# Optimization experiments

Hardware: AMD Instinct MI355X
Metric: run time of the kernel (lower is better)

The kernel has to match this reference:

```python
import jax, jax.numpy as jnp
import numpy as np

K = 20  # max_similar_relations


def setup_inputs() -> dict:
    key = jax.random.key(0)
    k1, k2 = jax.random.split(key)
    B, R, D = 256, 2048, 64
    x = jax.random.normal(k1, (B, R, D), dtype=jnp.float32)
    query_rels = jax.random.randint(k2, (B,), 0, R, dtype=jnp.int32)
    return {
        "x": x,
        "query_rels": query_rels,
        # raw params as in __init__: threshold_init=0.2 -> raw=0.2*2-1=-0.6; strength_init=0.05 -> raw=0.05*5-1=-0.75
        "threshold_raw": jnp.float32(-0.6),
        "strength_raw": jnp.float32(-0.75),
        "weight_scale": jnp.float32(1.0),
        "temperature": jnp.float32(1.0),
    }


def reference(x, query_rels, threshold_raw, strength_raw, weight_scale, temperature):
    B, R, D = x.shape
    bidx = jnp.arange(B)
    threshold = jax.nn.sigmoid(threshold_raw)
    strength = jax.nn.sigmoid(strength_raw) * 0.2
    temp = jnp.clip(temperature, 0.1, 10.0)

    # F.normalize(x, p=2, dim=2)
    norms = x / jnp.maximum(jnp.linalg.norm(x, axis=2, keepdims=True), 1e-12)

    q = norms[bidx, query_rels]                      # [B, D] normalized query reprs
    sims = jnp.einsum("bd,brd->br", q, norms)        # [B, R] cosine similarities
    sims = sims.at[bidx, query_rels].set(-1.0)       # exclude self
    sim_w = jax.nn.sigmoid((sims - threshold) * 10.0)

    topv, topi = jax.lax.top_k(sims, K)              # [B, K]
    valid = (topv > threshold) & (topi != query_rels[:, None])

    # softmax over valid top-k entries only (per batch row)
    logits = jnp.where(valid, topv / temp, -1e9)
    w = jax.nn.softmax(logits, axis=1)
    w = jnp.where(valid, w, 0.0)

    sw = jnp.take_along_axis(sim_w, topi, axis=1)    # smooth sigmoid weights of selected
    combined = w * sw
    adjusted = combined * (1.0 + weight_scale * topv)
    adjusted = adjusted / (jnp.sum(adjusted, axis=1, keepdims=True) + 1e-8)

    # gather top-k normalized reprs and weighted-sum them
    top_reprs = jnp.take_along_axis(norms, jnp.broadcast_to(topi[:, :, None], (B, K, D)), axis=1)
    weighted = jnp.einsum("bk,bkd->bd", adjusted, top_reprs)  # [B, D]

    q_orig = x[bidx, query_rels]                     # original (unnormalized) query repr
    has_valid = jnp.any(valid, axis=1, keepdims=True)
    mixed = (1.0 - strength) * q_orig + strength * weighted
    new_q = jnp.where(has_valid, mixed, q_orig)

    return x.at[bidx, query_rels].set(new_q)
```

## Files before the change

### kernel.cpp

```cpp
#include <hip/hip_runtime.h>
#include <math.h>

#define KTOP 20
#define R_MAX 2048
#define SPLIT 8

typedef float f4v __attribute__((ext_vector_type(4)));

__global__ __launch_bounds__(256, 6) void stream_sims(
    const float* __restrict__ x,
    const int* __restrict__ qrels,
    float* __restrict__ out,
    float* __restrict__ sims,
    float* __restrict__ dns,
    int R)
{
    __shared__ float s_q[64];
    const int blk = blockIdx.x;
    const int b = blk >> 3;
    const int s = blk & (SPLIT - 1);
    const int t = threadIdx.x;
    const int qr = qrels[b];
    const long xbase = (long)b * R * 64;

    if (t < 64) {
        float v = x[xbase + (long)qr * 64 + t];
        float ss = v * v;
#pragma unroll
        for (int m = 1; m < 64; m <<= 1) ss += __shfl_xor(ss, m, 64);
        s_q[t] = v / fmaxf(sqrtf(ss), 1e-12f);
    }
    __syncthreads();

    const int grp = t >> 4, l16 = t & 15;
    const float4 q4 = *(const float4*)(s_q + l16 * 4);
    const int rpb = R / SPLIT;
    const int row0 = s * rpb;
    const long sbase = (long)b * R;

    for (int r = row0 + grp; r < row0 + rpb; r += 32) {
        const int rA = r, rB = r + 16;
        const long baseA = xbase + (long)rA * 64 + l16 * 4;
        const long baseB = xbase + (long)rB * 64 + l16 * 4;
        const float4 vA = *(const float4*)(x + baseA);
        const float4 vB = *(const float4*)(x + baseB);
        __builtin_nontemporal_store(*(const f4v*)&vA, (f4v*)(out + baseA));
        __builtin_nontemporal_store(*(const f4v*)&vB, (f4v*)(out + baseB));

        float dotA = vA.x * q4.x + vA.y * q4.y + vA.z * q4.z + vA.w * q4.w;
        float ssA  = vA.x * vA.x + vA.y * vA.y + vA.z * vA.z + vA.w * vA.w;
        float dotB = vB.x * q4.x + vB.y * q4.y + vB.z * q4.z + vB.w * q4.w;
        float ssB  = vB.x * vB.x + vB.y * vB.y + vB.z * vB.z + vB.w * vB.w;
#pragma unroll
        for (int m = 1; m < 16; m <<= 1) {
            dotA += __shfl_xor(dotA, m, 64);
            ssA  += __shfl_xor(ssA,  m, 64);
            dotB += __shfl_xor(dotB, m, 64);
            ssB  += __shfl_xor(ssB,  m, 64);
        }
        if (l16 == 0) {
            float dnA = fmaxf(sqrtf(ssA), 1e-12f);
            float dnB = fmaxf(sqrtf(ssB), 1e-12f);
            sims[sbase + rA] = (rA == qr) ? -1.0f : dotA / dnA;
            sims[sbase + rB] = (rB == qr) ? -1.0f : dotB / dnB;
            dns[sbase + rA] = dnA;
            dns[sbase + rB] = dnB;
        }
    }
}

__global__ __launch_bounds__(256) void select_mix(
    const float* __restrict__ x,
    const int* __restrict__ qrels,
    const float* __restrict__ thr_raw,
    const float* __restrict__ str_raw,
    const float* __restrict__ wscale_p,
    const float* __restrict__ temp_p,
    const float* __restrict__ sims,
    const float* __restrict__ dns,
    float* __restrict__ out,
    int R)
{
    __shared__ float s_sims[R_MAX];
    __shared__ int   s_cand[R_MAX];
    __shared__ int   s_ncand;
    __shared__ float s_topv[KTOP];
    __shared__ int   s_topi[KTOP];
    __shared__ float s_dnsel[KTOP];
    __shared__ float s_adj[KTOP];
    __shared__ float s_strength;

    const int b = blockIdx.x;
    const int t = threadIdx.x;
    const int qr = qrels[b];
    const float threshold = 1.0f / (1.0f + expf(-thr_raw[0]));
    const long sbase = (long)b * R;
    const long xbase = (long)b * R * 64;

    if (t == 0) s_ncand = 0;
    __syncthreads();

    for (int i = t; i < R; i += 256) {
        float sv = sims[sbase + i];
        s_sims[i] = sv;
        if (sv > threshold) {
            int p = atomicAdd(&s_ncand, 1);
            s_cand[p] = i;
        }
    }
    __syncthreads();

    const int ncand = s_ncand;
    const int ksel = ncand < KTOP ? ncand : KTOP;

    if (t < 64) {
        float myv = 0.0f; int myi = 0;
        if (ncand > KTOP) {
            float lv[32]; int li[32];
#pragma unroll
            for (int j = 0; j < 32; ++j) {
                int i = t + 64 * j;
                if (i < ncand) { li[j] = s_cand[i]; lv[j] = s_sims[li[j]]; }
                else           { li[j] = 0x7fffffff; lv[j] = -INFINITY; }
            }
            for (int k = 0; k < KTOP; ++k) {
                float bv = -INFINITY; int bi = 0x7fffffff;
#pragma unroll
                for (int j = 0; j < 32; ++j)
                    if (lv[j] > bv || (lv[j] == bv && li[j] < bi)) { bv = lv[j]; bi = li[j]; }
#pragma unroll
                for (int m = 1; m < 64; m <<= 1) {
                    float v2 = __shfl_xor(bv, m, 64);
                    int   i2 = __shfl_xor(bi, m, 64);
                    if (v2 > bv || (v2 == bv && i2 < bi)) { bv = v2; bi = i2; }
                }
#pragma unroll
                for (int j = 0; j < 32; ++j) if (li[j] == bi) lv[j] = -INFINITY;
                if (t == k) { myv = bv; myi = bi; }
            }
        } else if (t < ksel) {
            myi = s_cand[t];
            myv = s_sims[myi];
        }
        if (t < ksel) {
            s_topv[t] = myv;
            s_topi[t] = myi;
            s_dnsel[t] = dns[sbase + myi];
        }
    }
    __syncthreads();

    if (t == 0) {
        float strength = (1.0f / (1.0f + expf(-str_raw[0]))) * 0.2f;
        float temp = fminf(fmaxf(temp_p[0], 0.1f), 10.0f);
        float wsc  = wscale_p[0];
        if (ksel > 0) {
            float m = -INFINITY;
            for (int k = 0; k < ksel; ++k) m = fmaxf(m, s_topv[k] / temp);
            float w[KTOP]; float wsum = 0.0f;
            for (int k = 0; k < ksel; ++k) { w[k] = expf(s_topv[k] / temp - m); wsum += w[k]; }
            float adj[KTOP]; float asum = 0.0f;
            for (int k = 0; k < ksel; ++k) {
                float tv = s_topv[k];
                float sw = 1.0f / (1.0f + expf(-(tv - threshold) * 10.0f));
                float a  = (w[k] / wsum) * sw * (1.0f + wsc * tv);
                adj[k] = a; asum += a;
            }
            for (int k = 0; k < ksel; ++k)
                s_adj[k] = (adj[k] / (asum + 1e-8f)) / s_dnsel[k];
        }
        s_strength = strength;
    }
    __syncthreads();

    if (t < 64 && ksel > 0) {
        const long qb = xbase + (long)qr * 64 + t;
        float qo = x[qb];
        float acc = 0.0f;
        for (int k = 0; k < ksel; ++k)
            acc += s_adj[k] * x[xbase + (long)s_topi[k] * 64 + t];
        float st = s_strength;
        out[qb] = (1.0f - st) * qo + st * acc;
    }
}

__global__ __launch_bounds__(1024) void fused_enhancer(
    const float* __restrict__ x,
    const int* __restrict__ qrels,
    const float* __restrict__ thr_raw,
    const float* __restrict__ str_raw,
    const float* __restrict__ wscale_p,
    const float* __restrict__ temp_p,
    float* __restrict__ out, int R)
{
    __shared__ float s_q[64];
    __shared__ float s_sims[R_MAX];
    __shared__ float s_dn[R_MAX];
    __shared__ int   s_cand[R_MAX];
    __shared__ int   s_ncand;
    __shared__ float s_topv[KTOP];
    __shared__ int   s_topi[KTOP];
    __shared__ float s_adj[KTOP];
    __shared__ float s_strength;

    const int b = blockIdx.x;
    const int t = threadIdx.x;
    const int qr = qrels[b];
    const float threshold = 1.0f / (1.0f + expf(-thr_raw[0]));

    if (t == 0) s_ncand = 0;

    if (t < 64) {
        float v = x[((long)b * R + qr) * 64 + t];
        float ss = v * v;
#pragma unroll
        for (int m = 1; m < 64; m <<= 1) ss += __shfl_xor(ss, m, 64);
        s_q[t] = v / fmaxf(sqrtf(ss), 1e-12f);
    }
    __syncthreads();

    const int grp = t >> 4, l16 = t & 15;
    const float4 q4 = *(const float4*)(s_q + l16 * 4);
    const long xbase = (long)b * R * 64;
    for (int row = grp; row < R; row += 64) {
        long base = xbase + (long)row * 64 + l16 * 4;
        const float4 v = *(const float4*)(x + base);
        *(float4*)(out + base) = v;
        float dot = v.x * q4.x + v.y * q4.y + v.z * q4.z + v.w * q4.w;
        float ss  = v.x * v.x + v.y * v.y + v.z * v.z + v.w * v.w;
#pragma unroll
        for (int m = 1; m < 16; m <<= 1) {
            dot += __shfl_xor(dot, m, 64);
            ss  += __shfl_xor(ss,  m, 64);
        }
        if (l16 == 0) {
            float dn  = fmaxf(sqrtf(ss), 1e-12f);
            float sim = (row == qr) ? -1.0f : dot / dn;
            s_sims[row] = sim;
            s_dn[row]   = dn;
            if (sim > threshold) {
                int p = atomicAdd(&s_ncand, 1);
                s_cand[p] = row;
            }
        }
    }
    __syncthreads();

    const int ncand = s_ncand;
    const int ksel = ncand < KTOP ? ncand : KTOP;

    if (t < 64) {
        if (ncand > KTOP) {
            float lv[32]; int li[32];
#pragma unroll
            for (int j = 0; j < 32; ++j) {
                int i = t + 64 * j;
                if (i < ncand) { li[j] = s_cand[i]; lv[j] = s_sims[li[j]]; }
                else           { li[j] = 0x7fffffff; lv[j] = -INFINITY; }
            }
            for (int k = 0; k < KTOP; ++k) {
                float bv = -INFINITY; int bi = 0x7fffffff;
#pragma unroll
                for (int j = 0; j < 32; ++j) {
                    if (lv[j] > bv || (lv[j] == bv && li[j] < bi)) { bv = lv[j]; bi = li[j]; }
                }
#pragma unroll
                for (int m = 1; m < 64; m <<= 1) {
                    float v2 = __shfl_xor(bv, m, 64);
                    int   i2 = __shfl_xor(bi, m, 64);
                    if (v2 > bv || (v2 == bv && i2 < bi)) { bv = v2; bi = i2; }
                }
#pragma unroll
                for (int j = 0; j < 32; ++j) if (li[j] == bi) lv[j] = -INFINITY;
                if (t == 0) { s_topv[k] = bv; s_topi[k] = bi; }
            }
        } else if (t == 0) {
            for (int k = 0; k < ksel; ++k) {
                int idx = s_cand[k];
                s_topi[k] = idx;
                s_topv[k] = s_sims[idx];
            }
        }
    }

    if (t == 0) {
        float strength = (1.0f / (1.0f + expf(-str_raw[0]))) * 0.2f;
        float temp = fminf(fmaxf(temp_p[0], 0.1f), 10.0f);
        float wsc  = wscale_p[0];
        if (ksel > 0) {
            float m = -INFINITY;
            for (int k = 0; k < ksel; ++k) m = fmaxf(m, s_topv[k] / temp);
            float w[KTOP]; float wsum = 0.0f;
            for (int k = 0; k < ksel; ++k) { w[k] = expf(s_topv[k] / temp - m); wsum += w[k]; }
            float adj[KTOP]; float asum = 0.0f;
            for (int k = 0; k < ksel; ++k) {
                float tv = s_topv[k];
                float sw = 1.0f / (1.0f + expf(-(tv - threshold) * 10.0f));
                float a  = (w[k] / wsum) * sw * (1.0f + wsc * tv);
                adj[k] = a; asum += a;
            }
            for (int k = 0; k < ksel; ++k)
                s_adj[k] = (adj[k] / (asum + 1e-8f)) / s_dn[s_topi[k]];
        }
        s_strength = strength;
    }
    __syncthreads();

    if (t < 64 && ksel > 0) {
        long qb = ((long)b * R + qr) * 64 + t;
        float qo = x[qb];
        float acc = 0.0f;
        for (int k = 0; k < ksel; ++k)
            acc += s_adj[k] * x[((long)b * R + s_topi[k]) * 64 + t];
        float st = s_strength;
        out[qb] = (1.0f - st) * qo + st * acc;
    }
}

extern "C" void kernel_launch(void* const* d_in, const int* in_sizes, int n_in,
                              void* d_out, int out_size, void* d_ws, size_t ws_size,
                              hipStream_t stream) {
    const float* x      = (const float*)d_in[0];
    const int*   qrels  = (const int*)d_in[1];
    const float* thr    = (const float*)d_in[2];
    const float* str    = (const float*)d_in[3];
    const float* wscale = (const float*)d_in[4];
    const float* temp   = (const float*)d_in[5];
    float* out = (float*)d_out;

    const int B = in_sizes[1];
    const int D = 64;
    const int R = in_sizes[0] / (B * D);
    (void)D;

    const size_t need = (size_t)B * R * 2 * sizeof(float);
    if (d_ws != nullptr && ws_size >= need && (R % (SPLIT * 32)) == 0 && R <= R_MAX) {
        float* sims = (float*)d_ws;
        float* dns  = sims + (size_t)B * R;
        stream_sims<<<B * SPLIT, 256, 0, stream>>>(x, qrels, out, sims, dns, R);
        select_mix<<<B, 256, 0, stream>>>(x, qrels, thr, str, wscale, temp,
                                          sims, dns, out, R);
    } else {
        fused_enhancer<<<B, 1024, 0, stream>>>(x, qrels, thr, str, wscale, temp, out, R);
    }
}
```

Before: 258.2 us.

## Transpose row tiles through LDS to replace shuffle reductions in similarity kernel

Rewrites the streaming similarity kernel so each wave loads 64 rows into registers up front, writes the copy to the output, and stages the rows through a padded LDS tile. Each lane then computes a full-row dot product and norm with one cross-half shuffle, replacing four-level shuffle reductions. It also drops the nontemporal stores and lowers the launch-bounds occupancy hint. The cost is extra LDS traffic and more register pressure, and the fast path now requires R to be a multiple of 2048.

```diff
diff --git a/kernel.cpp b/kernel.cpp
--- a/kernel.cpp
+++ b/kernel.cpp
@@ -4,10 +4,11 @@
 #define KTOP 20
 #define R_MAX 2048
 #define SPLIT 8
-
-typedef float f4v __attribute__((ext_vector_type(4)));
-
-__global__ __launch_bounds__(256, 6) void stream_sims(
+#define ST 66
+
+static_assert(sizeof(float) * (4 * 32 * ST + 64) < 36 * 1024, "LDS budget");
+
+__global__ __launch_bounds__(256, 3) void stream_sims(
     const float* __restrict__ x,
     const int* __restrict__ qrels,
     float* __restrict__ out,
@@ -16,12 +17,15 @@
     int R)
 {
     __shared__ float s_q[64];
+    __shared__ float s_tile[4][32 * ST];
+
     const int blk = blockIdx.x;
     const int b = blk >> 3;
     const int s = blk & (SPLIT - 1);
     const int t = threadIdx.x;
     const int qr = qrels[b];
     const long xbase = (long)b * R * 64;
+    const long sbase = (long)b * R;
 
     if (t < 64) {
         float v = x[xbase + (long)qr * 64 + t];
@@ -32,39 +36,82 @@
     }
     __syncthreads();
 
-    const int grp = t >> 4, l16 = t & 15;
-    const float4 q4 = *(const float4*)(s_q + l16 * 4);
-    const int rpb = R / SPLIT;
-    const int row0 = s * rpb;
-    const long sbase = (long)b * R;
-
-    for (int r = row0 + grp; r < row0 + rpb; r += 32) {
-        const int rA = r, rB = r + 16;
-        const long baseA = xbase + (long)rA * 64 + l16 * 4;
-        const long baseB = xbase + (long)rB * 64 + l16 * 4;
-        const float4 vA = *(const float4*)(x + baseA);
-        const float4 vB = *(const float4*)(x + baseB);
-        __builtin_nontemporal_store(*(const f4v*)&vA, (f4v*)(out + baseA));
-        __builtin_nontemporal_store(*(const f4v*)&vB, (f4v*)(out + baseB));
-
-        float dotA = vA.x * q4.x + vA.y * q4.y + vA.z * q4.z + vA.w * q4.w;
-        float ssA  = vA.x * vA.x + vA.y * vA.y + vA.z * vA.z + vA.w * vA.w;
-        float dotB = vB.x * q4.x + vB.y * q4.y + vB.z * q4.z + vB.w * q4.w;
-        float ssB  = vB.x * vB.x + vB.y * vB.y + vB.z * vB.z + vB.w * vB.w;
-#pragma unroll
-        for (int m = 1; m < 16; m <<= 1) {
-            dotA += __shfl_xor(dotA, m, 64);
-            ssA  += __shfl_xor(ssA,  m, 64);
-            dotB += __shfl_xor(dotB, m, 64);
-            ssB  += __shfl_xor(ssB,  m, 64);
-        }
-        if (l16 == 0) {
-            float dnA = fmaxf(sqrtf(ssA), 1e-12f);
-            float dnB = fmaxf(sqrtf(ssB), 1e-12f);
-            sims[sbase + rA] = (rA == qr) ? -1.0f : dotA / dnA;
-            sims[sbase + rB] = (rB == qr) ? -1.0f : dotB / dnB;
-            dns[sbase + rA] = dnA;
-            dns[sbase + rB] = dnB;
+    const int wid = t >> 6, lane = t & 63;
+    const int g4 = lane >> 4, l16 = lane & 15;
+    const int h = lane >> 5, l32 = lane & 31;
+
+    float4 q[8];
+#pragma unroll
+    for (int k = 0; k < 8; ++k) q[k] = *(const float4*)(s_q + h * 32 + k * 4);
+
+    const int row0 = s * (R / SPLIT) + wid * 64;
+    const int rA0 = row0, rB0 = row0 + 32;
+
+    float* lds = &s_tile[wid][0];
+
+    float4 vA[8], vB[8];
+#pragma unroll
+    for (int j = 0; j < 8; ++j)
+        vA[j] = *(const float4*)(x + xbase + (long)(rA0 + g4 + 4 * j) * 64 + l16 * 4);
+#pragma unroll
+    for (int j = 0; j < 8; ++j)
+        vB[j] = *(const float4*)(x + xbase + (long)(rB0 + g4 + 4 * j) * 64 + l16 * 4);
+
+#pragma unroll
+    for (int j = 0; j < 8; ++j) {
+        const int r = g4 + 4 * j;
+        *(float4*)(out + xbase + (long)(rA0 + r) * 64 + l16 * 4) = vA[j];
+        float* p = lds + r * ST + l16 * 4;
+        *(float2*)(p)     = make_float2(vA[j].x, vA[j].y);
+        *(float2*)(p + 2) = make_float2(vA[j].z, vA[j].w);
+    }
+    {
+        float dot = 0.0f, ssv = 0.0f;
+        const float* rp = lds + l32 * ST + h * 32;
+#pragma unroll
+        for (int k = 0; k < 16; ++k) {
+            float2 rv = *(const float2*)(rp + 2 * k);
+            const float* qf = (const float*)&q[k >> 1];
+            float qa = qf[(2 * k) & 3], qb = qf[(2 * k + 1) & 3];
+            dot += rv.x * qa + rv.y * qb;
+            ssv += rv.x * rv.x + rv.y * rv.y;
+        }
+        dot += __shfl_xor(dot, 32, 64);
+        ssv += __shfl_xor(ssv, 32, 64);
+        if (h == 0) {
+            const int row = rA0 + l32;
+            float dn = fmaxf(sqrtf(ssv), 1e-12f);
+            sims[sbase + row] = (row == qr) ? -1.0f : dot / dn;
+            dns[sbase + row] = dn;
+        }
+    }
+
+#pragma unroll
+    for (int j = 0; j < 8; ++j) {
+        const int r = g4 + 4 * j;
+        *(float4*)(out + xbase + (long)(rB0 + r) * 64 + l16 * 4) = vB[j];
+        float* p = lds + r * ST + l16 * 4;
+        *(float2*)(p)     = make_float2(vB[j].x, vB[j].y);
+        *(float2*)(p + 2) = make_float2(vB[j].z, vB[j].w);
+    }
+    {
+        float dot = 0.0f, ssv = 0.0f;
+        const float* rp = lds + l32 * ST + h * 32;
+#pragma unroll
+        for (int k = 0; k < 16; ++k) {
+            float2 rv = *(const float2*)(rp + 2 * k);
+            const float* qf = (const float*)&q[k >> 1];
+            float qa = qf[(2 * k) & 3], qb = qf[(2 * k + 1) & 3];
+            dot += rv.x * qa + rv.y * qb;
+            ssv += rv.x * rv.x + rv.y * rv.y;
+        }
+        dot += __shfl_xor(dot, 32, 64);
+        ssv += __shfl_xor(ssv, 32, 64);
+        if (h == 0) {
+            const int row = rB0 + l32;
+            float dn = fmaxf(sqrtf(ssv), 1e-12f);
+            sims[sbase + row] = (row == qr) ? -1.0f : dot / dn;
+            dns[sbase + row] = dn;
         }
     }
 }
@@ -334,7 +381,7 @@
     (void)D;
 
     const size_t need = (size_t)B * R * 2 * sizeof(float);
-    if (d_ws != nullptr && ws_size >= need && (R % (SPLIT * 32)) == 0 && R <= R_MAX) {
+    if (d_ws != nullptr && ws_size >= need && (R % (SPLIT * 256)) == 0 && R <= R_MAX) {
         float* sims = (float*)d_ws;
         float* dns  = sims + (size_t)B * R;
         stream_sims<<<B * SPLIT, 256, 0, stream>>>(x, qrels, out, sims, dns, R);
```

Result: faster. 252.2 us (-2.3%).

## Split output copy from similarity streaming and raise load-level parallelism

Applied to the files above, without the earlier changes.

The streaming kernel no longer writes the copy of x to the output. A separate grid-stride kernel now does that copy with nontemporal vector stores. The similarity kernel is restructured so each wave issues four independent row loads per iteration with a fully unrolled fixed trip count. This aims to increase memory-level parallelism and occupancy in each kernel, at the cost of reading x from memory a second time and adding an extra launch. The fast-path condition is tightened to R divisible by SPLIT*256.

```diff
diff --git a/kernel.cpp b/kernel.cpp
--- a/kernel.cpp
+++ b/kernel.cpp
@@ -7,21 +7,21 @@
 
 typedef float f4v __attribute__((ext_vector_type(4)));
 
-__global__ __launch_bounds__(256, 6) void stream_sims(
+__global__ __launch_bounds__(256, 8) void sims_only(
     const float* __restrict__ x,
     const int* __restrict__ qrels,
-    float* __restrict__ out,
     float* __restrict__ sims,
     float* __restrict__ dns,
     int R)
 {
     __shared__ float s_q[64];
-    const int blk = blockIdx.x;
-    const int b = blk >> 3;
-    const int s = blk & (SPLIT - 1);
+    const int idx = blockIdx.x;
+    const int b = idx >> 3;
+    const int s = idx & (SPLIT - 1);
     const int t = threadIdx.x;
     const int qr = qrels[b];
     const long xbase = (long)b * R * 64;
+    const long sbase = (long)b * R;
 
     if (t < 64) {
         float v = x[xbase + (long)qr * 64 + t];
@@ -32,41 +32,64 @@
     }
     __syncthreads();
 
-    const int grp = t >> 4, l16 = t & 15;
+    const int l16 = t & 15;
+    const int gw  = (t >> 4) & 3;
+    const int w   = t >> 6;
     const float4 q4 = *(const float4*)(s_q + l16 * 4);
-    const int rpb = R / SPLIT;
-    const int row0 = s * rpb;
-    const long sbase = (long)b * R;
-
-    for (int r = row0 + grp; r < row0 + rpb; r += 32) {
-        const int rA = r, rB = r + 16;
-        const long baseA = xbase + (long)rA * 64 + l16 * 4;
-        const long baseB = xbase + (long)rB * 64 + l16 * 4;
-        const float4 vA = *(const float4*)(x + baseA);
-        const float4 vB = *(const float4*)(x + baseB);
-        __builtin_nontemporal_store(*(const f4v*)&vA, (f4v*)(out + baseA));
-        __builtin_nontemporal_store(*(const f4v*)&vB, (f4v*)(out + baseB));
-
-        float dotA = vA.x * q4.x + vA.y * q4.y + vA.z * q4.z + vA.w * q4.w;
-        float ssA  = vA.x * vA.x + vA.y * vA.y + vA.z * vA.z + vA.w * vA.w;
-        float dotB = vB.x * q4.x + vB.y * q4.y + vB.z * q4.z + vB.w * q4.w;
-        float ssB  = vB.x * vB.x + vB.y * vB.y + vB.z * vB.z + vB.w * vB.w;
+
+    const int row0 = s * (R / SPLIT) + w * 64;
+
+#pragma unroll
+    for (int it = 0; it < 4; ++it) {
+        const int rbase = row0 + it * 16;
+        float4 v[4];
+#pragma unroll
+        for (int j = 0; j < 4; ++j)
+            v[j] = *(const float4*)(x + xbase + (long)(rbase + 4 * j + gw) * 64 + l16 * 4);
+        float dot[4], ssv[4];
+#pragma unroll
+        for (int j = 0; j < 4; ++j) {
+            dot[j] = v[j].x * q4.x + v[j].y * q4.y + v[j].z * q4.z + v[j].w * q4.w;
+            ssv[j] = v[j].x * v[j].x + v[j].y * v[j].y + v[j].z * v[j].z + v[j].w * v[j].w;
+        }
 #pragma unroll
         for (int m = 1; m < 16; m <<= 1) {
-            dotA += __shfl_xor(dotA, m, 64);
-            ssA  += __shfl_xor(ssA,  m, 64);
-            dotB += __shfl_xor(dotB, m, 64);
-            ssB  += __shfl_xor(ssB,  m, 64);
+#pragma unroll
+            for (int j = 0; j < 4; ++j) {
+                dot[j] += __shfl_xor(dot[j], m, 64);
+                ssv[j] += __shfl_xor(ssv[j], m, 64);
+            }
         }
         if (l16 == 0) {
-            float dnA = fmaxf(sqrtf(ssA), 1e-12f);
-            float dnB = fmaxf(sqrtf(ssB), 1e-12f);
-            sims[sbase + rA] = (rA == qr) ? -1.0f : dotA / dnA;
-            sims[sbase + rB] = (rB == qr) ? -1.0f : dotB / dnB;
-            dns[sbase + rA] = dnA;
-            dns[sbase + rB] = dnB;
-        }
-    }
+#pragma unroll
+            for (int j = 0; j < 4; ++j) {
+                const int row = rbase + 4 * j + gw;
+                float dn = fmaxf(sqrtf(ssv[j]), 1e-12f);
+                sims[sbase + row] = (row == qr) ? -1.0f : dot[j] / dn;
+                dns[sbase + row] = dn;
+            }
+        }
+    }
+}
+
+__global__ __launch_bounds__(256, 8) void copy_out(
+    const f4v* __restrict__ src,
+    f4v* __restrict__ dst,
+    long n4, long stride)
+{
+    long i = (long)blockIdx.x * 256 + threadIdx.x;
+    for (; i + 3 * stride < n4; i += 4 * stride) {
+        f4v a = src[i];
+        f4v b = src[i + stride];
+        f4v c = src[i + 2 * stride];
+        f4v d = src[i + 3 * stride];
+        __builtin_nontemporal_store(a, &dst[i]);
+        __builtin_nontemporal_store(b, &dst[i + stride]);
+        __builtin_nontemporal_store(c, &dst[i + 2 * stride]);
+        __builtin_nontemporal_store(d, &dst[i + 3 * stride]);
+    }
+    for (; i < n4; i += stride)
+        __builtin_nontemporal_store(src[i], &dst[i]);
 }
 
 __global__ __launch_bounds__(256) void select_mix(
@@ -334,10 +357,14 @@
     (void)D;
 
     const size_t need = (size_t)B * R * 2 * sizeof(float);
-    if (d_ws != nullptr && ws_size >= need && (R % (SPLIT * 32)) == 0 && R <= R_MAX) {
+    if (d_ws != nullptr && ws_size >= need && (R % (SPLIT * 256)) == 0 && R <= R_MAX) {
         float* sims = (float*)d_ws;
         float* dns  = sims + (size_t)B * R;
-        stream_sims<<<B * SPLIT, 256, 0, stream>>>(x, qrels, out, sims, dns, R);
+        const long n4 = (long)B * R * 16;
+        const int  cgrid = 2048;
+        const long cstride = (long)cgrid * 256;
+        sims_only<<<B * SPLIT, 256, 0, stream>>>(x, qrels, sims, dns, R);
+        copy_out<<<cgrid, 256, 0, stream>>>((const f4v*)x, (f4v*)out, n4, cstride);
         select_mix<<<B, 256, 0, stream>>>(x, qrels, thr, str, wscale, temp,
                                           sims, dns, out, R);
     } else {
```

Result: slower. 274.9 us (+6.5%).
